# Performance work log

Measured on AMD Instinct MI355X. Metric: run time of the kernel, lower is better.

The kernel has to match this reference:

```python
import jax, jax.numpy as jnp
import numpy as np

B, S, D = 4, 2048, 1024
H = 2 * D          # hidden_dim = 2*n_embd
A = H // 16        # adapt_dim = 128
E = 8              # num_experts
K = 2              # top-k within group
GS = 4             # group_size
G = E // GS        # num_groups


def _ln(x, g, b, eps=1e-5):
    m = x.mean(-1, keepdims=True)
    v = x.var(-1, keepdims=True)
    return (x - m) / jnp.sqrt(v + eps) * g + b


def setup_inputs() -> dict:
    key = jax.random.key(0)
    ks = jax.random.split(key, 12)
    s = 1.0 / np.sqrt(D)       # shared MLP init scale
    sa = s * 0.01              # adapt layers init scale
    se = 0.01 / np.sqrt(A)     # expert adapter init scale
    f32 = jnp.float32
    return {
        "x": jax.random.normal(ks[0], (B, S, D), f32),
        "W_up": jax.random.normal(ks[1], (H, D), f32) * s,
        "W_gate": jax.random.normal(ks[2], (H, D), f32) * s,
        "W_down": jax.random.normal(ks[3], (D, H), f32) * s,
        "W_pre": jax.random.normal(ks[4], (A, D), f32) * sa,
        "W_post": jax.random.normal(ks[5], (A, H), f32) * sa,
        "g_an": jnp.ones((A,), f32),
        "b_an": jnp.zeros((A,), f32),
        "W_aproj": jax.random.normal(ks[6], (H, A), f32) * sa,
        "W_eadapt": jax.random.normal(ks[7], (E, A, A), f32) * se,
        "g_e": jnp.ones((E, A), f32),
        "b_e": jnp.zeros((E, A), f32),
        "W_eproj": jax.random.normal(ks[8], (H, A), f32) * se,
        "W_oproj": jax.random.normal(ks[9], (D, H), f32) * se,
        "W_rg": jax.random.normal(ks[10], (G, D), f32) * 0.001,
        "W_re": jax.random.normal(ks[11], (GS, D), f32) * 0.001,
    }


def reference(x, W_up, W_gate, W_down, W_pre, W_post, g_an, b_an, W_aproj,
              W_eadapt, g_e, b_e, W_eproj, W_oproj, W_rg, W_re):
    Bs, Ss, Ds = x.shape
    N = Bs * Ss
    xf = x.reshape(N, Ds)

    # ---- HierarchicalRouter ----
    gl = xf @ W_rg.T                                   # [N, G]
    gp = jax.nn.softmax(gl, axis=-1)
    gw = gp.max(axis=-1)                               # top-1 group weight
    gi = gp.argmax(axis=-1)                            # top-1 group index
    ll = xf @ W_re.T                                   # [N, GS]
    lp = jax.nn.softmax(ll, axis=-1)
    lw, li = jax.lax.top_k(lp, K)                      # [N, K]
    eidx = gi[:, None] * GS + li                       # global expert ids
    lw = lw / (lw.sum(-1, keepdims=True) + 1e-7)
    fw = gw[:, None] * lw                              # final weights [N, K]
    dispatch = jnp.zeros((N, E), x.dtype).at[jnp.arange(N)[:, None], eidx].set(fw)
    load = dispatch.sum(0)
    target = load.sum() / E
    load_balance_loss = jnp.mean((load - target) ** 2)
    z_loss = jnp.mean(gl ** 2) + jnp.mean(ll ** 2)
    router_loss = 0.001 * (load_balance_loss + z_loss)

    # ---- SharedExpertMLP ----
    up = x @ W_up.T                                    # [B, S, H]
    gate = x @ W_gate.T
    hidden = jax.nn.silu(gate) * up
    pre = x @ W_pre.T                                  # [B, S, A]
    a_in = _ln(pre, g_an, b_an)
    a_out = _ln(hidden @ W_post.T, g_an, b_an)
    aw = jax.nn.silu(jnp.clip(jnp.einsum('bsa,bta->bst', a_in, a_out), -5.0, 5.0))
    adapt = jnp.einsum('bst,bta->bsa', aw, a_in) @ W_aproj.T  # [B, S, H]
    hidden = hidden + 0.1 * adapt
    shared = hidden @ W_down.T                         # [B, S, D]

    # ---- ExpertGroup (vectorized gather/MLP/scatter) ----
    # sum_i w_i * (shared + 0.1*contrib_i) = shared*sum(w) + 0.1*sum_i w_i*contrib_i
    w = dispatch.reshape(Bs, Ss, E)                    # dispatch weights
    he = jnp.einsum('bsa,eca->ebsc', pre, W_eadapt)    # [E, B, S, A]
    he = _ln(he, g_e[:, None, None, :], b_e[:, None, None, :])
    wh = jnp.einsum('ebsa,bse->bsa', he, w)            # weighted combine at adapt_dim
    contrib = (wh @ W_eproj.T) @ W_oproj.T             # [B, S, D]
    out = shared * w.sum(-1, keepdims=True) + 0.1 * contrib
    return out, router_loss
```

## Files before the change

### kernel.cpp

```cpp
#include <hip/hip_runtime.h>
#include <hip/hip_bf16.h>

typedef unsigned short u16;
typedef short bf16x8 __attribute__((ext_vector_type(8)));
typedef float f32x4 __attribute__((ext_vector_type(4)));

#define N_TOK 8192
#define DIM   1024
#define HID   2048
#define ADIM  128
#define SEQ   2048
#define LDP   2304

__device__ __forceinline__ u16 f2bf_bits(float f){
  unsigned u = __float_as_uint(f);
  unsigned r = (u + 0x7fffu + ((u >> 16) & 1u)) >> 16;
  return (u16)r;
}
__device__ __forceinline__ float bf2f(u16 v){ return __uint_as_float((unsigned)v << 16); }
__device__ __forceinline__ float siluf(float x){ return x / (1.f + __expf(-x)); }

__device__ __forceinline__ void gload16(const void* g, void* l){
  __builtin_amdgcn_global_load_lds((const __attribute__((address_space(1))) void*)g,
                                   (__attribute__((address_space(3))) void*)l, 16, 0, 0);
}

#define SB0() __builtin_amdgcn_sched_barrier(0)

__global__ void __launch_bounds__(512, 2)
gemm_gu256(const u16* __restrict__ X, const u16* __restrict__ Wgu,
           const float* __restrict__ sumw, u16* __restrict__ hidP)
{
  extern __shared__ u16 lds[];
  const int tid = threadIdx.x, w = tid >> 6, lane = tid & 63;
  const int wm = w >> 2, wn = w & 3;
  const int xcd = blockIdx.x & 7, lloc = blockIdx.x >> 3;
  const int bm = (xcd >> 1) * 8 + (lloc & 7);
  const int bn = (xcd & 1) * 8 + (lloc >> 3);
  const long brow = (long)bm * 256, bcol = (long)bn * 256;
  const int frow = lane & 15;
  const int fks = ((lane >> 4) * 8) ^ (((lane >> 1) & 3) << 3);
  const int srow = lane >> 2;
  const int sslot = (((lane & 3) ^ ((lane >> 3) & 3)) * 8);

  f32x4 acc[8][4];
  #pragma unroll
  for (int m = 0; m < 8; m++)
    #pragma unroll
    for (int n = 0; n < 4; n++)
      #pragma unroll
      for (int i = 0; i < 4; i++) acc[m][n][i] = 0.f;

  auto stage = [&](const u16* __restrict__ gbase, long row0, int kt, int kh,
                   int p, int regoff) {
    #pragma unroll
    for (int i = 0; i < 2; i++) {
      const int r = (i * 8 + w) * 16 + srow;
      const u16* g = gbase + (row0 + r) * 1024 + kt * 64 + kh * 32 + sslot;
      u16* l = &lds[p * 32768 + regoff + kh * 8192 + (i * 8 + w) * 512];
      gload16(g, l);
    }
  };

#define AFRAG(mf, kss) (*(const bf16x8*)&lds[p*32768 + (kss)*8192 + (wm*128 + (mf)*16 + frow)*32 + fks])
#define BFRAG(nf, kss) (*(const bf16x8*)&lds[p*32768 + 16384 + (kss)*8192 + (wn*64 + (nf)*16 + frow)*32 + fks])

  stage(X, brow, 0, 0, 0, 0);
  stage(Wgu, bcol, 0, 0, 0, 16384);
  stage(X, brow, 0, 1, 0, 0);
  stage(Wgu, bcol, 0, 1, 0, 16384);
  asm volatile("s_waitcnt vmcnt(4)" ::: "memory");
  __builtin_amdgcn_s_barrier();

  for (int kt = 0; kt < 16; ++kt) {
    const int p = kt & 1, pn = p ^ 1;
    const int ktn = (kt < 15) ? kt + 1 : 15;
    bf16x8 b[4], a[4];

    a[0] = AFRAG(0, 0);
    b[0] = BFRAG(0, 0); b[1] = BFRAG(1, 0); b[2] = BFRAG(2, 0); b[3] = BFRAG(3, 0);
    SB0();
    a[1] = AFRAG(1, 0); SB0();
    a[2] = AFRAG(2, 0); SB0();
    a[3] = AFRAG(3, 0);
    stage(X, brow, ktn, 0, pn, 0);
    __builtin_amdgcn_s_barrier();
    asm volatile("s_waitcnt lgkmcnt(3)" ::: "memory"); SB0();
    __builtin_amdgcn_s_setprio(1);
    #pragma unroll
    for (int n = 0; n < 4; n++)
      acc[0][n] = __builtin_amdgcn_mfma_f32_16x16x32_bf16(a[0], b[n], acc[0][n], 0, 0, 0);
    asm volatile("s_waitcnt lgkmcnt(2)" ::: "memory"); SB0();
    #pragma unroll
    for (int n = 0; n < 4; n++)
      acc[1][n] = __builtin_amdgcn_mfma_f32_16x16x32_bf16(a[1], b[n], acc[1][n], 0, 0, 0);
    asm volatile("s_waitcnt lgkmcnt(1)" ::: "memory"); SB0();
    #pragma unroll
    for (int n = 0; n < 4; n++)
      acc[2][n] = __builtin_amdgcn_mfma_f32_16x16x32_bf16(a[2], b[n], acc[2][n], 0, 0, 0);
    asm volatile("s_waitcnt lgkmcnt(0)" ::: "memory"); SB0();
    #pragma unroll
    for (int n = 0; n < 4; n++)
      acc[3][n] = __builtin_amdgcn_mfma_f32_16x16x32_bf16(a[3], b[n], acc[3][n], 0, 0, 0);
    __builtin_amdgcn_s_setprio(0);
    __builtin_amdgcn_s_barrier();

    a[0] = AFRAG(4, 0); SB0();
    a[1] = AFRAG(5, 0); SB0();
    a[2] = AFRAG(6, 0); SB0();
    a[3] = AFRAG(7, 0);
    stage(Wgu, bcol, ktn, 0, pn, 16384);
    __builtin_amdgcn_s_barrier();
    asm volatile("s_waitcnt lgkmcnt(3)" ::: "memory"); SB0();
    __builtin_amdgcn_s_setprio(1);
    #pragma unroll
    for (int n = 0; n < 4; n++)
      acc[4][n] = __builtin_amdgcn_mfma_f32_16x16x32_bf16(a[0], b[n], acc[4][n], 0, 0, 0);
    asm volatile("s_waitcnt lgkmcnt(2)" ::: "memory"); SB0();
    #pragma unroll
    for (int n = 0; n < 4; n++)
      acc[5][n] = __builtin_amdgcn_mfma_f32_16x16x32_bf16(a[1], b[n], acc[5][n], 0, 0, 0);
    asm volatile("s_waitcnt lgkmcnt(1)" ::: "memory"); SB0();
    #pragma unroll
    for (int n = 0; n < 4; n++)
      acc[6][n] = __builtin_amdgcn_mfma_f32_16x16x32_bf16(a[2], b[n], acc[6][n], 0, 0, 0);
    asm volatile("s_waitcnt lgkmcnt(0)" ::: "memory"); SB0();
    #pragma unroll
    for (int n = 0; n < 4; n++)
      acc[7][n] = __builtin_amdgcn_mfma_f32_16x16x32_bf16(a[3], b[n], acc[7][n], 0, 0, 0);
    __builtin_amdgcn_s_setprio(0);
    asm volatile("s_waitcnt vmcnt(4)" ::: "memory");
    __builtin_amdgcn_s_barrier();

    a[0] = AFRAG(0, 1);
    b[0] = BFRAG(0, 1); b[1] = BFRAG(1, 1); b[2] = BFRAG(2, 1); b[3] = BFRAG(3, 1);
    SB0();
    a[1] = AFRAG(1, 1); SB0();
    a[2] = AFRAG(2, 1); SB0();
    a[3] = AFRAG(3, 1);
    stage(X, brow, ktn, 1, pn, 0);
    __builtin_amdgcn_s_barrier();
    asm volatile("s_waitcnt lgkmcnt(3)" ::: "memory"); SB0();
    __builtin_amdgcn_s_setprio(1);
    #pragma unroll
    for (int n = 0; n < 4; n++)
      acc[0][n] = __builtin_amdgcn_mfma_f32_16x16x32_bf16(a[0], b[n], acc[0][n], 0, 0, 0);
    asm volatile("s_waitcnt lgkmcnt(2)" ::: "memory"); SB0();
    #pragma unroll
    for (int n = 0; n < 4; n++)
      acc[1][n] = __builtin_amdgcn_mfma_f32_16x16x32_bf16(a[1], b[n], acc[1][n], 0, 0, 0);
    asm volatile("s_waitcnt lgkmcnt(1)" ::: "memory"); SB0();
    #pragma unroll
    for (int n = 0; n < 4; n++)
      acc[2][n] = __builtin_amdgcn_mfma_f32_16x16x32_bf16(a[2], b[n], acc[2][n], 0, 0, 0);
    asm volatile("s_waitcnt lgkmcnt(0)" ::: "memory"); SB0();
    #pragma unroll
    for (int n = 0; n < 4; n++)
      acc[3][n] = __builtin_amdgcn_mfma_f32_16x16x32_bf16(a[3], b[n], acc[3][n], 0, 0, 0);
    __builtin_amdgcn_s_setprio(0);
    __builtin_amdgcn_s_barrier();

    a[0] = AFRAG(4, 1); SB0();
    a[1] = AFRAG(5, 1); SB0();
    a[2] = AFRAG(6, 1); SB0();
    a[3] = AFRAG(7, 1);
    stage(Wgu, bcol, ktn, 1, pn, 16384);
    __builtin_amdgcn_s_barrier();
    asm volatile("s_waitcnt lgkmcnt(3)" ::: "memory"); SB0();
    __builtin_amdgcn_s_setprio(1);
    #pragma unroll
    for (int n = 0; n < 4; n++)
      acc[4][n] = __builtin_amdgcn_mfma_f32_16x16x32_bf16(a[0], b[n], acc[4][n], 0, 0, 0);
    asm volatile("s_waitcnt lgkmcnt(2)" ::: "memory"); SB0();
    #pragma unroll
    for (int n = 0; n < 4; n++)
      acc[5][n] = __builtin_amdgcn_mfma_f32_16x16x32_bf16(a[1], b[n], acc[5][n], 0, 0, 0);
    asm volatile("s_waitcnt lgkmcnt(1)" ::: "memory"); SB0();
    #pragma unroll
    for (int n = 0; n < 4; n++)
      acc[6][n] = __builtin_amdgcn_mfma_f32_16x16x32_bf16(a[2], b[n], acc[6][n], 0, 0, 0);
    asm volatile("s_waitcnt lgkmcnt(0)" ::: "memory"); SB0();
    #pragma unroll
    for (int n = 0; n < 4; n++)
      acc[7][n] = __builtin_amdgcn_mfma_f32_16x16x32_bf16(a[3], b[n], acc[7][n], 0, 0, 0);
    __builtin_amdgcn_s_setprio(0);
    asm volatile("s_waitcnt vmcnt(4)" ::: "memory");
    __builtin_amdgcn_s_barrier();
  }
#undef AFRAG
#undef BFRAG

  #pragma unroll
  for (int mf = 0; mf < 8; mf++)
    #pragma unroll
    for (int i = 0; i < 4; i++) {
      const long r = brow + wm * 128 + mf * 16 + (lane >> 4) * 4 + i;
      const float sw = sumw[r];
      #pragma unroll
      for (int q = 0; q < 2; q++) {
        const float g = acc[mf][2 * q][i], u = acc[mf][2 * q + 1][i];
        const int hcol = (bn * 8 + wn * 2 + q) * 16 + (lane & 15);
        hidP[r * LDP + hcol] = f2bf_bits(sw * (siluf(g) * u));
      }
    }
}

__device__ __forceinline__ void kloop128(const u16* __restrict__ A, const u16* __restrict__ B,
                                         int lda, int ldb, int K,
                                         u16* lA, u16* lB, f32x4 (&acc)[4][4])
{
  const int tid = threadIdx.x, wave = tid >> 6, lane = tid & 63;
  const int wr = (wave >> 1) * 64, wc = (wave & 1) * 64;
  const int sr = tid >> 2, sks = ((tid & 3) ^ ((tid >> 3) & 3)) * 8;
  const u16* gA = A + (long)sr * lda + sks;
  const u16* gB = B + (long)sr * ldb + sks;
  const long rA = (long)64 * lda, rB = (long)64 * ldb;
  u16* lA0 = &lA[wave * 512]; u16* lA1 = &lA[2048 + wave * 512];
  u16* lB0 = &lB[wave * 512]; u16* lB1 = &lB[2048 + wave * 512];
  const int frow = lane & 15;
  const int fks = ((lane >> 4) * 8) ^ (((lane >> 1) & 3) << 3);

  for (int kt = 0; kt < K; kt += 32) {
    gload16(gA, lA0); gload16(gA + rA, lA1);
    gload16(gB, lB0); gload16(gB + rB, lB1);
    gA += 32; gB += 32;
    asm volatile("s_waitcnt vmcnt(0)" ::: "memory");
    __syncthreads();
    bf16x8 af[4], bfv[4];
    #pragma unroll
    for (int m = 0; m < 4; m++) af[m] = *(const bf16x8*)&lA[(wr + m * 16 + frow) * 32 + fks];
    #pragma unroll
    for (int n = 0; n < 4; n++) bfv[n] = *(const bf16x8*)&lB[(wc + n * 16 + frow) * 32 + fks];
    #pragma unroll
    for (int m = 0; m < 4; m++)
      #pragma unroll
      for (int n = 0; n < 4; n++)
        acc[m][n] = __builtin_amdgcn_mfma_f32_16x16x32_bf16(af[m], bfv[n], acc[m][n], 0, 0, 0);
    __syncthreads();
  }
}

__device__ __forceinline__ void acc_zero(f32x4 (&acc)[4][4]){
  #pragma unroll
  for (int m = 0; m < 4; m++)
    #pragma unroll
    for (int n = 0; n < 4; n++)
      #pragma unroll
      for (int i = 0; i < 4; i++) acc[m][n][i] = 0.f;
}

#define FA_AIN 0
#define FA_S   4096
#define FA_AO  8192
#define FA_AI  40960
__global__ void __launch_bounds__(256, 2)
fused_adapt(const u16* __restrict__ a_in, const u16* __restrict__ a_inT,
            const u16* __restrict__ a_out, const float* __restrict__ sumw,
            u16* __restrict__ hidP)
{
  extern __shared__ u16 lds[];
  const int tid = threadIdx.x, w = tid >> 6, lane = tid & 63;
  const int l15 = lane & 15, khi = lane >> 4;
  const int b = blockIdx.x >> 6, yt = blockIdx.x & 63;
  const int n0 = yt * 32;
  const u16* ain_b  = a_in  + (long)b * SEQ * ADIM;
  const u16* aout_b = a_out + (long)b * SEQ * ADIM;
  const u16* ainT_b = a_inT + (long)b * ADIM * SEQ;

  #pragma unroll
  for (int k = 0; k < 2; k++) {
    int c = tid + k * 256;
    int row = c >> 4, slot = c & 15;
    gload16(ain_b + (long)(n0 + row) * ADIM + ((slot ^ (row & 7)) * 8),
            &lds[FA_AIN + c * 8]);
  }
  auto stage_tile = [&](int t0, int pb) {
    #pragma unroll
    for (int k = 0; k < 8; k++) {
      int c = tid + k * 256;
      int row = c >> 4, slot = c & 15;
      gload16(aout_b + (long)(t0 + row) * ADIM + ((slot ^ (row & 7)) * 8),
              &lds[FA_AO + pb * 16384 + c * 8]);
    }
    #pragma unroll
    for (int k = 0; k < 8; k++) {
      int c = tid + k * 256;
      int row = c >> 4, slot = c & 15;
      gload16(ainT_b + (long)row * SEQ + t0 + ((slot ^ (row & 7)) * 8),
              &lds[FA_AI + pb * 16384 + c * 8]);
    }
  };
  stage_tile(0, 0);

  f32x4 pacc[2][2];
  #pragma unroll
  for (int mr = 0; mr < 2; mr++)
    #pragma unroll
    for (int nc = 0; nc < 2; nc++)
      #pragma unroll
      for (int i = 0; i < 4; i++) pacc[mr][nc][i] = 0.f;

#define LF(base, row, kc) (*(const bf16x8*)&lds[(base) + (row)*128 + (((kc) ^ ((row)&7)) * 8)])
#define MF(a_, b_, c_) __builtin_amdgcn_mfma_f32_16x16x32_bf16(a_, b_, c_, 0, 0, 0)

  for (int tt = 0; tt < 16; ++tt) {
    const int p = tt & 1;
    const int ttn = (tt < 15) ? tt + 1 : 15;
    stage_tile(ttn * 128, p ^ 1);
    asm volatile("s_waitcnt vmcnt(16)" ::: "memory");
    __syncthreads();

    f32x4 sacc[2][2];
    #pragma unroll
    for (int mr = 0; mr < 2; mr++)
      #pragma unroll
      for (int nc = 0; nc < 2; nc++)
        #pragma unroll
        for (int i = 0; i < 4; i++) sacc[mr][nc][i] = 0.f;
    const int AOb = FA_AO + p * 16384;
    #pragma unroll
    for (int ks = 0; ks < 4; ks++) {
      int kc = ks * 4 + khi;
      bf16x8 a0 = LF(FA_AIN, l15, kc);
      bf16x8 a1 = LF(FA_AIN, 16 + l15, kc);
      bf16x8 b0 = LF(AOb, w * 32 + l15, kc);
      bf16x8 b1 = LF(AOb, w * 32 + 16 + l15, kc);
      sacc[0][0] = MF(a0, b0, sacc[0][0]);
      sacc[0][1] = MF(a0, b1, sacc[0][1]);
      sacc[1][0] = MF(a1, b0, sacc[1][0]);
      sacc[1][1] = MF(a1, b1, sacc[1][1]);
    }
    #pragma unroll
    for (int mr = 0; mr < 2; mr++)
      #pragma unroll
      for (int nc = 0; nc < 2; nc++)
        #pragma unroll
        for (int i = 0; i < 4; i++) {
          int row = mr * 16 + khi * 4 + i;
          int col = w * 32 + nc * 16 + l15;
          float v = fminf(5.f, fmaxf(-5.f, sacc[mr][nc][i]));
          lds[FA_S + row * 128 + (((col >> 3) ^ (row & 7)) * 8) + (col & 7)] =
              f2bf_bits(siluf(v));
        }
    __syncthreads();
    const int AIb = FA_AI + p * 16384;
    #pragma unroll
    for (int ks = 0; ks < 4; ks++) {
      int kc = ks * 4 + khi;
      bf16x8 a0 = LF(FA_S, l15, kc);
      bf16x8 a1 = LF(FA_S, 16 + l15, kc);
      bf16x8 b0 = LF(AIb, w * 32 + l15, kc);
      bf16x8 b1 = LF(AIb, w * 32 + 16 + l15, kc);
      pacc[0][0] = MF(a0, b0, pacc[0][0]);
      pacc[0][1] = MF(a0, b1, pacc[0][1]);
      pacc[1][0] = MF(a1, b0, pacc[1][0]);
      pacc[1][1] = MF(a1, b1, pacc[1][1]);
    }
    __syncthreads();
  }
#undef LF
#undef MF

  const long nb = (long)b * SEQ + n0;
  #pragma unroll
  for (int mr = 0; mr < 2; mr++)
    #pragma unroll
    for (int nc = 0; nc < 2; nc++)
      #pragma unroll
      for (int i = 0; i < 4; i++) {
        long n = nb + mr * 16 + khi * 4 + i;
        int c = w * 32 + nc * 16 + l15;
        hidP[n * LDP + 2048 + c] = f2bf_bits(0.1f * sumw[n] * pacc[mr][nc][i]);
      }
}

__global__ void __launch_bounds__(256, 2)
split_pq(const u16* __restrict__ xb, const u16* __restrict__ Wpreb,
         const u16* __restrict__ WdQ, const u16* __restrict__ WaTb,
         const u16* __restrict__ Wob, const u16* __restrict__ WeTb,
         float* __restrict__ part, float* __restrict__ qpart)
{
  __shared__ u16 lA[4096];
  __shared__ u16 lB[4096];
  const int blk = blockIdx.x;
  const int wave = threadIdx.x >> 6, lane = threadIdx.x & 63;
  f32x4 acc[4][4]; acc_zero(acc);
  const int wr = (wave >> 1) * 64, wc = (wave & 1) * 64;

  if (blk < 256) {
    const int y = blk & 63, z = blk >> 6;
    const long brow = (long)y * 128;
    const u16* A = xb + brow * DIM + (long)z * 256;
    const u16* B = Wpreb + (long)z * 256;
    kloop128(A, B, DIM, DIM, 256, lA, lB, acc);
    float* po = part + (long)z * (N_TOK * ADIM);
    const long rr = brow + wr + ((lane >> 4) << 2);
    const int cc = wc + (lane & 15);
    #pragma unroll
    for (int m = 0; m < 4; m++)
      #pragma unroll
      for (int i = 0; i < 4; i++) {
        long r = rr + m * 16 + i;
        #pragma unroll
        for (int n = 0; n < 4; n++)
          po[r * 128 + cc + n * 16] = acc[m][n][i];
      }
  } else {
    const int q = blk - 256;
    const int y = q & 7, z = q >> 3;
    const int sel = z >> 2, split = z & 3;
    const long brow = (long)y * 128;
    const int lda = sel ? HID : LDP;
    const u16* A = (sel ? Wob : WdQ) + brow * lda + (long)split * 512;
    const u16* B = (sel ? WeTb : WaTb) + (long)split * 512;
    kloop128(A, B, lda, HID, 512, lA, lB, acc);
    float* po = qpart + (long)z * 131072;
    const long rr = brow + wr + ((lane >> 4) << 2);
    const int cc = wc + (lane & 15);
    #pragma unroll
    for (int m = 0; m < 4; m++)
      #pragma unroll
      for (int i = 0; i < 4; i++) {
        long r = rr + m * 16 + i;
        #pragma unroll
        for (int n = 0; n < 4; n++)
          po[r * 128 + cc + n * 16] = acc[m][n][i];
      }
  }
}

__global__ void __launch_bounds__(256, 2)
he_postf(const u16* __restrict__ preb, const u16* __restrict__ Weadb,
         u16* __restrict__ heb, const u16* __restrict__ hidP,
         const u16* __restrict__ Wpostb, float* __restrict__ postfp)
{
  __shared__ u16 lA[4096];
  __shared__ u16 lB[4096];
  const int blk = blockIdx.x;
  const int wave = threadIdx.x >> 6, lane = threadIdx.x & 63;
  f32x4 acc[4][4]; acc_zero(acc);
  const int wr = (wave >> 1) * 64, wc = (wave & 1) * 64;

  if (blk < 512) {
    const int y = blk & 63, e = blk >> 6;
    const long brow = (long)y * 128;
    const u16* A = preb + brow * ADIM;
    const u16* B = Weadb + (long)e * ADIM * ADIM;
    kloop128(A, B, ADIM, ADIM, ADIM, lA, lB, acc);
    u16* O = heb + (long)e * N_TOK * ADIM;
    const long r0 = brow + wr + ((lane >> 4) << 2);
    const long c0 = wc + (lane & 15);
    #pragma unroll
    for (int m = 0; m < 4; m++)
      #pragma unroll
      for (int i = 0; i < 4; i++) {
        long r = r0 + m * 16 + i;
        #pragma unroll
        for (int n = 0; n < 4; n++)
          O[r * ADIM + c0 + n * 16] = f2bf_bits(acc[m][n][i]);
      }
  } else {
    const int q = blk - 512;
    const int y = q & 63, z = q >> 6;
    const long brow = (long)y * 128;
    const u16* A = hidP + brow * LDP + (long)z * 512;
    const u16* B = Wpostb + (long)z * 512;
    kloop128(A, B, LDP, HID, 512, lA, lB, acc);
    float* po = postfp + (long)z * (N_TOK * ADIM);
    const long rr = brow + wr + ((lane >> 4) << 2);
    const int cc = wc + (lane & 15);
    #pragma unroll
    for (int m = 0; m < 4; m++)
      #pragma unroll
      for (int i = 0; i < 4; i++) {
        long r = rr + m * 16 + i;
        #pragma unroll
        for (int n = 0; n < 4; n++)
          po[r * 128 + cc + n * 16] = acc[m][n][i];
      }
  }
}

__global__ void __launch_bounds__(256, 2)
gemm_f32(const u16* __restrict__ Ag, const u16* __restrict__ Bg,
         const float* __restrict__ stats, float* __restrict__ out)
{
  __shared__ u16 lA[4096];
  __shared__ u16 lB[4096];
  const int wave = threadIdx.x >> 6, lane = threadIdx.x & 63;
  const long brow = (long)blockIdx.y * 128, bcol = (long)blockIdx.x * 128;
  f32x4 acc[4][4]; acc_zero(acc);
  kloop128(Ag + brow * LDP, Bg + bcol * LDP, LDP, LDP, LDP, lA, lB, acc);
  const int wr = (wave >> 1) * 64, wc = (wave & 1) * 64;
  const long r0 = brow + wr + ((lane >> 4) << 2);
  const long c0 = bcol + wc + (lane & 15);
  #pragma unroll
  for (int m = 0; m < 4; m++)
    #pragma unroll
    for (int i = 0; i < 4; i++) {
      long r = r0 + m * 16 + i;
      #pragma unroll
      for (int n = 0; n < 4; n++)
        out[r * DIM + c0 + n * 16] = acc[m][n][i];
    }
  if (blockIdx.x == 0 && blockIdx.y == 0 && threadIdx.x == 0) {
    float tot = 0;
    #pragma unroll
    for (int e = 0; e < 8; e++) tot += stats[e];
    float target = tot * 0.125f;
    float lb = 0;
    #pragma unroll
    for (int e = 0; e < 8; e++) { float d = stats[e] - target; lb += d * d; }
    lb *= 0.125f;
    float z = stats[8] * (1.f / (8192.f * 2.f)) + stats[9] * (1.f / (8192.f * 4.f));
    out[(size_t)N_TOK * DIM] = 0.001f * (lb + z);
  }
}

__global__ void __launch_bounds__(256)
prep_all(const float* __restrict__ x, const float* __restrict__ Wrg,
         const float* __restrict__ Wre, float* __restrict__ sumw,
         float* __restrict__ fwv, int* __restrict__ eidxv,
         float* __restrict__ stats, u16* __restrict__ xb,
         const float* __restrict__ Wg, const float* __restrict__ Wu,
         const float* __restrict__ Wd, const float* __restrict__ Wo,
         const float* __restrict__ Wpost, const float* __restrict__ Wpre,
         const float* __restrict__ Wead,
         u16* __restrict__ Wgu, u16* __restrict__ WdQ,
         u16* __restrict__ Wob, u16* __restrict__ Wpostb,
         u16* __restrict__ Wpreb, u16* __restrict__ Weadb,
         const float* __restrict__ Wa, const float* __restrict__ We,
         u16* __restrict__ Ta, u16* __restrict__ Te)
{
  __shared__ float lst[10];
  const int blk = blockIdx.x;
  if (blk < 512) {
    if (threadIdx.x < 10) lst[threadIdx.x] = 0.f;
    __syncthreads();
    const int wave = threadIdx.x >> 6, lane = threadIdx.x & 63;
    const float4* wg0 = (const float4*)Wrg;
    const float4* wg1 = (const float4*)(Wrg + 1024);
    const float4* we0 = (const float4*)Wre;
    const float4* we1 = (const float4*)(Wre + 1024);
    const float4* we2 = (const float4*)(Wre + 2048);
    const float4* we3 = (const float4*)(Wre + 3072);
    for (int t = 0; t < 4; t++) {
      const long n = (long)blk * 16 + wave * 4 + t;
      const float4* xr = (const float4*)(x + n * 1024);
      float d0 = 0, d1 = 0, t0 = 0, t1 = 0, t2 = 0, t3 = 0;
      #pragma unroll
      for (int j = 0; j < 4; j++) {
        int id = j * 64 + lane;
        float4 xv = xr[id];
        ushort4 xc;
        xc.x = f2bf_bits(xv.x); xc.y = f2bf_bits(xv.y);
        xc.z = f2bf_bits(xv.z); xc.w = f2bf_bits(xv.w);
        *(ushort4*)(xb + n * 1024 + id * 4) = xc;
        float4 a;
        a = wg0[id]; d0 += xv.x * a.x + xv.y * a.y + xv.z * a.z + xv.w * a.w;
        a = wg1[id]; d1 += xv.x * a.x + xv.y * a.y + xv.z * a.z + xv.w * a.w;
        a = we0[id]; t0 += xv.x * a.x + xv.y * a.y + xv.z * a.z + xv.w * a.w;
        a = we1[id]; t1 += xv.x * a.x + xv.y * a.y + xv.z * a.z + xv.w * a.w;
        a = we2[id]; t2 += xv.x * a.x + xv.y * a.y + xv.z * a.z + xv.w * a.w;
        a = we3[id]; t3 += xv.x * a.x + xv.y * a.y + xv.z * a.z + xv.w * a.w;
      }
      #pragma unroll
      for (int o = 32; o; o >>= 1) {
        d0 += __shfl_xor(d0, o); d1 += __shfl_xor(d1, o);
        t0 += __shfl_xor(t0, o); t1 += __shfl_xor(t1, o);
        t2 += __shfl_xor(t2, o); t3 += __shfl_xor(t3, o);
      }
      if (lane == 0) {
        float mg = fmaxf(d0, d1);
        float e0 = __expf(d0 - mg), e1 = __expf(d1 - mg);
        float invg = 1.f / (e0 + e1);
        float p0 = e0 * invg, p1 = e1 * invg;
        int gi = (d1 > d0) ? 1 : 0;
        float gw = fmaxf(p0, p1);
        float l[4] = {t0, t1, t2, t3};
        float ml = fmaxf(fmaxf(l[0], l[1]), fmaxf(l[2], l[3]));
        float p[4]; float su = 0;
        #pragma unroll
        for (int i = 0; i < 4; i++) { p[i] = __expf(l[i] - ml); su += p[i]; }
        float isu = 1.f / su;
        #pragma unroll
        for (int i = 0; i < 4; i++) p[i] *= isu;
        int i1 = 0;
        #pragma unroll
        for (int i = 1; i < 4; i++) if (p[i] > p[i1]) i1 = i;
        int i2 = (i1 == 0) ? 1 : 0;
        #pragma unroll
        for (int i = 0; i < 4; i++) if (i != i1 && p[i] > p[i2]) i2 = i;
        float s2 = p[i1] + p[i2];
        float invs = 1.f / (s2 + 1e-7f);
        float f1 = gw * p[i1] * invs, f2 = gw * p[i2] * invs;
        int ea = gi * 4 + i1, eb = gi * 4 + i2;
        sumw[n] = f1 + f2;
        fwv[2 * n] = f1; fwv[2 * n + 1] = f2;
        eidxv[2 * n] = ea; eidxv[2 * n + 1] = eb;
        atomicAdd(&lst[ea], f1);
        atomicAdd(&lst[eb], f2);
        atomicAdd(&lst[8], d0 * d0 + d1 * d1);
        atomicAdd(&lst[9], t0 * t0 + t1 * t1 + t2 * t2 + t3 * t3);
      }
    }
    __syncthreads();
    if (threadIdx.x < 10) atomicAdd(&stats[threadIdx.x], lst[threadIdx.x]);
  } else if (blk < 4864) {
    long i = ((long)(blk - 512) * 256 + threadIdx.x) * 8;
    const float* s; u16* d; long so, doff;
    if (i < 4194304) {
      long rp = i >> 10, c = i & 1023;
      long i32 = rp >> 5, wi = rp & 31;
      s = (wi < 16) ? Wg : Wu;
      so = (i32 * 16 + (wi & 15)) * 1024 + c;
      d = Wgu; doff = i;
    } else if (i < 6291456) {
      long j = i - 4194304;
      long r = j >> 11, c = j & 2047;
      s = Wd; so = j;
      d = WdQ; doff = r * LDP + c;
    } else if (i < 8388608) { s = Wo;    so = i - 6291456; d = Wob;    doff = so; }
    else if (i < 8650752)   { s = Wpost; so = i - 8388608; d = Wpostb; doff = so; }
    else if (i < 8781824)   { s = Wpre;  so = i - 8650752; d = Wpreb;  doff = so; }
    else                    { s = Wead;  so = i - 8781824; d = Weadb;  doff = so; }
    float4 v0 = *(const float4*)(s + so), v1 = *(const float4*)(s + so + 4);
    ushort4 p, q;
    p.x = f2bf_bits(v0.x); p.y = f2bf_bits(v0.y); p.z = f2bf_bits(v0.z); p.w = f2bf_bits(v0.w);
    q.x = f2bf_bits(v1.x); q.y = f2bf_bits(v1.y); q.z = f2bf_bits(v1.z); q.w = f2bf_bits(v1.w);
    *(ushort4*)(d + doff) = p;
    *(ushort4*)(d + doff + 4) = q;
  } else {
    int bid = blk - 4864;
    const float* src = (bid < 1024) ? Wa : We;
    u16* dst = (bid < 1024) ? Ta : Te;
    int idx = (bid & 1023) * 256 + threadIdx.x;
    int c = idx >> 11, r = idx & 2047;
    dst[idx] = f2bf_bits(src[(long)r * 128 + c]);
  }
}

__global__ void __launch_bounds__(256)
ln1_rq(const float* __restrict__ part, const float* __restrict__ qpart,
       const float* __restrict__ g, const float* __restrict__ b,
       u16* __restrict__ a_in, u16* __restrict__ a_inT, u16* __restrict__ preb,
       u16* __restrict__ WdQ)
{
  const int blk = blockIdx.x;
  if (blk < 2048) {
    int wave = threadIdx.x >> 6, lane = threadIdx.x & 63;
    long n = (long)blk * 4 + wave;
    long base = n * 128;
    float x0 = 0.f, x1 = 0.f;
    #pragma unroll
    for (int s = 0; s < 4; s++) {
      x0 += part[(long)s * (N_TOK * ADIM) + base + lane];
      x1 += part[(long)s * (N_TOK * ADIM) + base + 64 + lane];
    }
    float s2 = x0 + x1, q = x0 * x0 + x1 * x1;
    #pragma unroll
    for (int o = 32; o; o >>= 1) { s2 += __shfl_xor(s2, o); q += __shfl_xor(q, o); }
    float m = s2 * (1.f / 128.f);
    float var = q * (1.f / 128.f) - m * m;
    float inv = rsqrtf(var + 1e-5f);
    float y0 = (x0 - m) * inv * g[lane] + b[lane];
    float y1 = (x1 - m) * inv * g[lane + 64] + b[lane + 64];
    a_in[base + lane] = f2bf_bits(y0);
    a_in[base + 64 + lane] = f2bf_bits(y1);
    long bb = n >> 11, ss = n & 2047;
    a_inT[(bb * 128 + lane) * 2048 + ss] = f2bf_bits(y0);
    a_inT[(bb * 128 + lane + 64) * 2048 + ss] = f2bf_bits(y1);
    preb[base + lane] = f2bf_bits(x0);
    preb[base + 64 + lane] = f2bf_bits(x1);
  } else {
    int idx = (blk - 2048) * 256 + threadIdx.x;
    int r = idx >> 8, c = idx & 255;
    const float* p = qpart + ((c < 128) ? 0 : 524288) + (long)r * 128 + (c & 127);
    float a = p[0] + p[131072] + p[262144] + p[393216];
    WdQ[(long)r * LDP + 2048 + c] = f2bf_bits(a);
  }
}

__global__ void __launch_bounds__(256)
lnc_ln2(const u16* __restrict__ heb, const int* __restrict__ eidxv,
        const float* __restrict__ fwv, const float* __restrict__ g_e,
        const float* __restrict__ b_e, u16* __restrict__ hidP,
        const float* __restrict__ postfp, const float* __restrict__ g_an,
        const float* __restrict__ b_an, const float* __restrict__ sumw,
        u16* __restrict__ a_out)
{
  const int blk = blockIdx.x;
  const int wave = threadIdx.x >> 6, lane = threadIdx.x & 63;
  if (blk < 2048) {
    const long n = (long)blk * 4 + wave;
    float o0 = 0.f, o1 = 0.f;
    #pragma unroll
    for (int k = 0; k < 2; k++) {
      const int e = eidxv[2 * n + k];
      const float w = fwv[2 * n + k];
      const u16* row = heb + ((long)e * N_TOK + n) * 128;
      float h0 = bf2f(row[lane]), h1 = bf2f(row[lane + 64]);
      float s = h0 + h1, q = h0 * h0 + h1 * h1;
      #pragma unroll
      for (int o = 32; o; o >>= 1) { s += __shfl_xor(s, o); q += __shfl_xor(q, o); }
      float m = s * (1.f / 128.f);
      float var = q * (1.f / 128.f) - m * m;
      float inv = rsqrtf(var + 1e-5f);
      o0 += w * ((h0 - m) * inv * g_e[e * 128 + lane] + b_e[e * 128 + lane]);
      o1 += w * ((h1 - m) * inv * g_e[e * 128 + lane + 64] + b_e[e * 128 + lane + 64]);
    }
    hidP[n * LDP + 2176 + lane] = f2bf_bits(0.1f * o0);
    hidP[n * LDP + 2176 + 64 + lane] = f2bf_bits(0.1f * o1);
  } else {
    long n = (long)(blk - 2048) * 4 + wave;
    long base = n * 128;
    float x0 = 0.f, x1 = 0.f;
    #pragma unroll
    for (int s = 0; s < 4; s++) {
      x0 += postfp[(long)s * (N_TOK * ADIM) + base + lane];
      x1 += postfp[(long)s * (N_TOK * ADIM) + base + 64 + lane];
    }
    float invw = 1.f / sumw[n]; x0 *= invw; x1 *= invw;
    float s2 = x0 + x1, q = x0 * x0 + x1 * x1;
    #pragma unroll
    for (int o = 32; o; o >>= 1) { s2 += __shfl_xor(s2, o); q += __shfl_xor(q, o); }
    float m = s2 * (1.f / 128.f);
    float var = q * (1.f / 128.f) - m * m;
    float inv = rsqrtf(var + 1e-5f);
    a_out[base + lane] = f2bf_bits((x0 - m) * inv * g_an[lane] + b_an[lane]);
    a_out[base + 64 + lane] = f2bf_bits((x1 - m) * inv * g_an[lane + 64] + b_an[lane + 64]);
  }
}

extern "C" void kernel_launch(void* const* d_in, const int* in_sizes, int n_in,
                              void* d_out, int out_size, void* d_ws, size_t ws_size,
                              hipStream_t stream)
{
  (void)in_sizes; (void)n_in; (void)out_size; (void)ws_size;
  const float* x       = (const float*)d_in[0];
  const float* W_up    = (const float*)d_in[1];
  const float* W_gate  = (const float*)d_in[2];
  const float* W_down  = (const float*)d_in[3];
  const float* W_pre   = (const float*)d_in[4];
  const float* W_post  = (const float*)d_in[5];
  const float* g_an    = (const float*)d_in[6];
  const float* b_an    = (const float*)d_in[7];
  const float* W_aproj = (const float*)d_in[8];
  const float* W_ead   = (const float*)d_in[9];
  const float* g_e     = (const float*)d_in[10];
  const float* b_e     = (const float*)d_in[11];
  const float* W_eproj = (const float*)d_in[12];
  const float* W_oproj = (const float*)d_in[13];
  const float* W_rg    = (const float*)d_in[14];
  const float* W_re    = (const float*)d_in[15];
  float* out = (float*)d_out;

  char* base = (char*)d_ws; size_t off = 0;
  auto alloc = [&](size_t bytes) -> void* {
    void* p = base + off; off = (off + bytes + 255) & ~(size_t)255; return p;
  };
  u16*   xb     = (u16*)  alloc((size_t)N_TOK * DIM * 2);
  u16*   Wgu    = (u16*)  alloc((size_t)2 * HID * DIM * 2);
  u16*   WdQ    = (u16*)  alloc((size_t)DIM * LDP * 2);
  u16*   Wob    = (u16*)  alloc((size_t)DIM * HID * 2);
  u16*   Wpostb = (u16*)  alloc((size_t)ADIM * HID * 2);
  u16*   Wpreb  = (u16*)  alloc((size_t)ADIM * DIM * 2);
  u16*   WaTb   = (u16*)  alloc((size_t)ADIM * HID * 2);
  u16*   WeTb   = (u16*)  alloc((size_t)ADIM * HID * 2);
  u16*   Weadb  = (u16*)  alloc((size_t)8 * ADIM * ADIM * 2);
  u16*   hidP   = (u16*)  alloc((size_t)N_TOK * LDP * 2);
  u16*   heb    = (u16*)  alloc((size_t)8 * N_TOK * ADIM * 2);
  float* part   = (float*)heb;
  u16*   preb   = (u16*)  alloc((size_t)N_TOK * ADIM * 2);
  u16*   a_in   = (u16*)  alloc((size_t)N_TOK * ADIM * 2);
  u16*   a_inT  = (u16*)  alloc((size_t)N_TOK * ADIM * 2);
  u16*   a_out  = (u16*)  alloc((size_t)N_TOK * ADIM * 2);
  float* sumw   = (float*)alloc((size_t)N_TOK * 4);
  float* fwv    = (float*)alloc((size_t)N_TOK * 2 * 4);
  int*   eidxv  = (int*)  alloc((size_t)N_TOK * 2 * 4);
  float* stats  = (float*)alloc(64);
  float* postfp = (float*)d_out;
  float* qpart  = (float*)((char*)d_out + 16777216);

  hipFuncSetAttribute((const void*)gemm_gu256,
                      hipFuncAttributeMaxDynamicSharedMemorySize, 131072);
  hipFuncSetAttribute((const void*)fused_adapt,
                      hipFuncAttributeMaxDynamicSharedMemorySize, 147456);

  hipMemsetAsync(stats, 0, 64, stream);

  prep_all<<<6912, 256, 0, stream>>>(x, W_rg, W_re, sumw, fwv, eidxv, stats, xb,
                                     W_gate, W_up, W_down, W_oproj, W_post, W_pre,
                                     W_ead, Wgu, WdQ, Wob, Wpostb, Wpreb, Weadb,
                                     W_aproj, W_eproj, WaTb, WeTb);

  gemm_gu256<<<512, 512, 131072, stream>>>(xb, Wgu, sumw, hidP);

  split_pq<<<320, 256, 0, stream>>>(xb, Wpreb, WdQ, WaTb, Wob, WeTb, part, qpart);

  ln1_rq<<<3072, 256, 0, stream>>>(part, qpart, g_an, b_an, a_in, a_inT, preb, WdQ);

  he_postf<<<768, 256, 0, stream>>>(preb, Weadb, heb, hidP, Wpostb, postfp);

  lnc_ln2<<<4096, 256, 0, stream>>>(heb, eidxv, fwv, g_e, b_e, hidP,
                                    postfp, g_an, b_an, sumw, a_out);

  fused_adapt<<<256, 256, 147456, stream>>>(a_in, a_inT, a_out, sumw, hidP);

  gemm_f32<<<dim3(8, 64, 1), 256, 0, stream>>>(hidP, WdQ, stats, out);
}
```

Measured before the change: 244.9 us.

## Halve fused_adapt row tile to double grid, and XCD-swizzle final GEMM blocks

```diff
diff --git a/kernel.cpp b/kernel.cpp
--- a/kernel.cpp
+++ b/kernel.cpp
@@ -249,10 +249,10 @@
       for (int i = 0; i < 4; i++) acc[m][n][i] = 0.f;
 }
 
-#define FA_AIN 0
-#define FA_S   4096
-#define FA_AO  8192
-#define FA_AI  40960
+#define FB_AIN 0
+#define FB_S   2048
+#define FB_AO  3072
+#define FB_AI  19456
 __global__ void __launch_bounds__(256, 2)
 fused_adapt(const u16* __restrict__ a_in, const u16* __restrict__ a_inT,
             const u16* __restrict__ a_out, const float* __restrict__ sumw,
@@ -261,117 +261,98 @@
   extern __shared__ u16 lds[];
   const int tid = threadIdx.x, w = tid >> 6, lane = tid & 63;
   const int l15 = lane & 15, khi = lane >> 4;
-  const int b = blockIdx.x >> 6, yt = blockIdx.x & 63;
-  const int n0 = yt * 32;
+  const int b = blockIdx.x >> 7, yt = blockIdx.x & 127;
+  const int n0 = yt * 16;
   const u16* ain_b  = a_in  + (long)b * SEQ * ADIM;
   const u16* aout_b = a_out + (long)b * SEQ * ADIM;
   const u16* ainT_b = a_inT + (long)b * ADIM * SEQ;
 
-  #pragma unroll
-  for (int k = 0; k < 2; k++) {
-    int c = tid + k * 256;
-    int row = c >> 4, slot = c & 15;
+  {
+    int c = tid, row = c >> 4, slot = c & 15;
     gload16(ain_b + (long)(n0 + row) * ADIM + ((slot ^ (row & 7)) * 8),
-            &lds[FA_AIN + c * 8]);
+            &lds[FB_AIN + c * 8]);
   }
   auto stage_tile = [&](int t0, int pb) {
     #pragma unroll
-    for (int k = 0; k < 8; k++) {
+    for (int k = 0; k < 4; k++) {
       int c = tid + k * 256;
       int row = c >> 4, slot = c & 15;
       gload16(aout_b + (long)(t0 + row) * ADIM + ((slot ^ (row & 7)) * 8),
-              &lds[FA_AO + pb * 16384 + c * 8]);
-    }
-    #pragma unroll
-    for (int k = 0; k < 8; k++) {
+              &lds[FB_AO + pb * 8192 + c * 8]);
+    }
+    #pragma unroll
+    for (int k = 0; k < 4; k++) {
       int c = tid + k * 256;
-      int row = c >> 4, slot = c & 15;
+      int row = c >> 3, slot = c & 7;
       gload16(ainT_b + (long)row * SEQ + t0 + ((slot ^ (row & 7)) * 8),
-              &lds[FA_AI + pb * 16384 + c * 8]);
+              &lds[FB_AI + pb * 8192 + c * 8]);
     }
   };
   stage_tile(0, 0);
 
-  f32x4 pacc[2][2];
+  f32x4 pacc[2];
   #pragma unroll
-  for (int mr = 0; mr < 2; mr++)
-    #pragma unroll
-    for (int nc = 0; nc < 2; nc++)
-      #pragma unroll
-      for (int i = 0; i < 4; i++) pacc[mr][nc][i] = 0.f;
-
-#define LF(base, row, kc) (*(const bf16x8*)&lds[(base) + (row)*128 + (((kc) ^ ((row)&7)) * 8)])
+  for (int nf = 0; nf < 2; nf++)
+    #pragma unroll
+    for (int i = 0; i < 4; i++) pacc[nf][i] = 0.f;
+
+#define LF256(base, row, kc) (*(const bf16x8*)&lds[(base) + (row)*128 + (((kc) ^ ((row)&7))*8)])
+#define LF128(base, row, kc) (*(const bf16x8*)&lds[(base) + (row)*64  + (((kc) ^ ((row)&7))*8)])
 #define MF(a_, b_, c_) __builtin_amdgcn_mfma_f32_16x16x32_bf16(a_, b_, c_, 0, 0, 0)
 
-  for (int tt = 0; tt < 16; ++tt) {
+  for (int tt = 0; tt < 32; ++tt) {
     const int p = tt & 1;
-    const int ttn = (tt < 15) ? tt + 1 : 15;
-    stage_tile(ttn * 128, p ^ 1);
-    asm volatile("s_waitcnt vmcnt(16)" ::: "memory");
+    const int ttn = (tt < 31) ? tt + 1 : 31;
+    stage_tile(ttn * 64, p ^ 1);
+    asm volatile("s_waitcnt vmcnt(8)" ::: "memory");
     __syncthreads();
 
-    f32x4 sacc[2][2];
-    #pragma unroll
-    for (int mr = 0; mr < 2; mr++)
-      #pragma unroll
-      for (int nc = 0; nc < 2; nc++)
-        #pragma unroll
-        for (int i = 0; i < 4; i++) sacc[mr][nc][i] = 0.f;
-    const int AOb = FA_AO + p * 16384;
+    f32x4 sacc;
+    #pragma unroll
+    for (int i = 0; i < 4; i++) sacc[i] = 0.f;
+    const int AOb = FB_AO + p * 8192;
     #pragma unroll
     for (int ks = 0; ks < 4; ks++) {
       int kc = ks * 4 + khi;
-      bf16x8 a0 = LF(FA_AIN, l15, kc);
-      bf16x8 a1 = LF(FA_AIN, 16 + l15, kc);
-      bf16x8 b0 = LF(AOb, w * 32 + l15, kc);
-      bf16x8 b1 = LF(AOb, w * 32 + 16 + l15, kc);
-      sacc[0][0] = MF(a0, b0, sacc[0][0]);
-      sacc[0][1] = MF(a0, b1, sacc[0][1]);
-      sacc[1][0] = MF(a1, b0, sacc[1][0]);
-      sacc[1][1] = MF(a1, b1, sacc[1][1]);
-    }
-    #pragma unroll
-    for (int mr = 0; mr < 2; mr++)
-      #pragma unroll
-      for (int nc = 0; nc < 2; nc++)
-        #pragma unroll
-        for (int i = 0; i < 4; i++) {
-          int row = mr * 16 + khi * 4 + i;
-          int col = w * 32 + nc * 16 + l15;
-          float v = fminf(5.f, fmaxf(-5.f, sacc[mr][nc][i]));
-          lds[FA_S + row * 128 + (((col >> 3) ^ (row & 7)) * 8) + (col & 7)] =
-              f2bf_bits(siluf(v));
-        }
+      bf16x8 av = LF256(FB_AIN, l15, kc);
+      bf16x8 bv = LF256(AOb, w * 16 + l15, kc);
+      sacc = MF(av, bv, sacc);
+    }
+    #pragma unroll
+    for (int i = 0; i < 4; i++) {
+      int row = khi * 4 + i;
+      int col = w * 16 + l15;
+      float v = fminf(5.f, fmaxf(-5.f, sacc[i]));
+      lds[FB_S + row * 64 + (((col >> 3) ^ (row & 7)) * 8) + (col & 7)] =
+          f2bf_bits(siluf(v));
+    }
     __syncthreads();
-    const int AIb = FA_AI + p * 16384;
-    #pragma unroll
-    for (int ks = 0; ks < 4; ks++) {
+    const int AIb = FB_AI + p * 8192;
+    #pragma unroll
+    for (int ks = 0; ks < 2; ks++) {
       int kc = ks * 4 + khi;
-      bf16x8 a0 = LF(FA_S, l15, kc);
-      bf16x8 a1 = LF(FA_S, 16 + l15, kc);
-      bf16x8 b0 = LF(AIb, w * 32 + l15, kc);
-      bf16x8 b1 = LF(AIb, w * 32 + 16 + l15, kc);
-      pacc[0][0] = MF(a0, b0, pacc[0][0]);
-      pacc[0][1] = MF(a0, b1, pacc[0][1]);
-      pacc[1][0] = MF(a1, b0, pacc[1][0]);
-      pacc[1][1] = MF(a1, b1, pacc[1][1]);
+      bf16x8 av = LF128(FB_S, l15, kc);
+      #pragma unroll
+      for (int nf = 0; nf < 2; nf++) {
+        bf16x8 bv = LF128(AIb, w * 32 + nf * 16 + l15, kc);
+        pacc[nf] = MF(av, bv, pacc[nf]);
+      }
     }
     __syncthreads();
   }
-#undef LF
+#undef LF256
+#undef LF128
 #undef MF
 
   const long nb = (long)b * SEQ + n0;
   #pragma unroll
-  for (int mr = 0; mr < 2; mr++)
-    #pragma unroll
-    for (int nc = 0; nc < 2; nc++)
-      #pragma unroll
-      for (int i = 0; i < 4; i++) {
-        long n = nb + mr * 16 + khi * 4 + i;
-        int c = w * 32 + nc * 16 + l15;
-        hidP[n * LDP + 2048 + c] = f2bf_bits(0.1f * sumw[n] * pacc[mr][nc][i]);
-      }
+  for (int nf = 0; nf < 2; nf++)
+    #pragma unroll
+    for (int i = 0; i < 4; i++) {
+      long n = nb + khi * 4 + i;
+      int c = w * 32 + nf * 16 + l15;
+      hidP[n * LDP + 2048 + c] = f2bf_bits(0.1f * sumw[n] * pacc[nf][i]);
+    }
 }
 
 __global__ void __launch_bounds__(256, 2)
@@ -488,7 +469,10 @@
   __shared__ u16 lA[4096];
   __shared__ u16 lB[4096];
   const int wave = threadIdx.x >> 6, lane = threadIdx.x & 63;
-  const long brow = (long)blockIdx.y * 128, bcol = (long)blockIdx.x * 128;
+  const int id = blockIdx.x;
+  const int xcd = id & 7, k = id >> 3;
+  const long brow = (long)(xcd * 8 + (k & 7)) * 128;
+  const long bcol = (long)(k >> 3) * 128;
   f32x4 acc[4][4]; acc_zero(acc);
   kloop128(Ag + brow * LDP, Bg + bcol * LDP, LDP, LDP, LDP, lA, lB, acc);
   const int wr = (wave >> 1) * 64, wc = (wave & 1) * 64;
@@ -503,7 +487,7 @@
       for (int n = 0; n < 4; n++)
         out[r * DIM + c0 + n * 16] = acc[m][n][i];
     }
-  if (blockIdx.x == 0 && blockIdx.y == 0 && threadIdx.x == 0) {
+  if (id == 0 && threadIdx.x == 0) {
     float tot = 0;
     #pragma unroll
     for (int e = 0; e < 8; e++) tot += stats[e];
@@ -785,7 +769,7 @@
   hipFuncSetAttribute((const void*)gemm_gu256,
                       hipFuncAttributeMaxDynamicSharedMemorySize, 131072);
   hipFuncSetAttribute((const void*)fused_adapt,
-                      hipFuncAttributeMaxDynamicSharedMemorySize, 147456);
+                      hipFuncAttributeMaxDynamicSharedMemorySize, 71680);
 
   hipMemsetAsync(stats, 0, 64, stream);
 
@@ -805,7 +789,7 @@
   lnc_ln2<<<4096, 256, 0, stream>>>(heb, eidxv, fwv, g_e, b_e, hidP,
                                     postfp, g_an, b_an, sumw, a_out);
 
-  fused_adapt<<<256, 256, 147456, stream>>>(a_in, a_inT, a_out, sumw, hidP);
-
-  gemm_f32<<<dim3(8, 64, 1), 256, 0, stream>>>(hidP, WdQ, stats, out);
-}
+  fused_adapt<<<512, 256, 71680, stream>>>(a_in, a_inT, a_out, sumw, hidP);
+
+  gemm_f32<<<512, 256, 0, stream>>>(hidP, WdQ, stats, out);
+}
```

New measurement: 240.8 us, median of 2. Within noise of the previous version (-1.7%).
